# Optimization experiments

Hardware: AMD Instinct MI355X
Metric: run time of the kernel (lower is better)

## Reference

```python
import jax, jax.numpy as jnp
import numpy as np

# CSSA config (index=0): H=W=64, strip windows h_spa=64, w_spa=8, heads=4, C=64
B, HW, C, HEADS = 32, 64, 64, 4
HS, WS = 64, 8          # h_spa, w_spa
HD = C // HEADS          # head_dim = 16
WIN = HS * WS            # 512 tokens per window
SCALE = HD ** -0.5


def setup_inputs() -> dict:
    key = jax.random.key(0)
    k1, k2, k3 = jax.random.split(key, 3)
    qkv = jax.random.normal(k1, (3, B, HW * HW, C), dtype=jnp.float32)
    w_conv = jax.random.normal(k2, (C, 1, 3, 3), dtype=jnp.float32) * 0.1
    b_conv = jax.random.normal(k3, (C,), dtype=jnp.float32) * 0.1
    return {"qkv": qkv, "w_conv": w_conv, "b_conv": b_conv}


def _to_img(x):
    # [B, N, C] -> [B, C, H, W]
    return jnp.transpose(x.reshape(B, HW, HW, C), (0, 3, 1, 2))


def _img2window_heads(x):
    img = _to_img(x)
    img = img.reshape(B, C, HW // HS, HS, HW // WS, WS)
    win = jnp.transpose(img, (0, 2, 4, 3, 5, 1)).reshape(-1, WIN, C)
    return jnp.transpose(win.reshape(-1, WIN, HEADS, HD), (0, 2, 1, 3))


def _v_windows(x):
    # [B, N, C] -> [B*nWin, C, h_spa, w_spa] (image-layout windows for conv)
    img = _to_img(x)
    img = img.reshape(B, C, HW // HS, HS, HW // WS, WS)
    return jnp.transpose(img, (0, 2, 4, 1, 3, 5)).reshape(-1, C, HS, WS)


def reference(qkv, w_conv, b_conv):
    q, k, v = qkv[0], qkv[1], qkv[2]
    qh = _img2window_heads(q) * SCALE
    kh = _img2window_heads(k)
    vw = _v_windows(v)                           # [Bw, C, HS, WS]
    # depthwise 3x3 conv LePE
    lepe = jax.lax.conv_general_dilated(
        vw, w_conv, window_strides=(1, 1), padding=((1, 1), (1, 1)),
        feature_group_count=C,
        dimension_numbers=("NCHW", "OIHW", "NCHW")) + b_conv[None, :, None, None]
    Bw = vw.shape[0]
    lepe = jnp.transpose(lepe.reshape(Bw, HEADS, HD, WIN), (0, 1, 3, 2))
    vh = jnp.transpose(vw.reshape(Bw, HEADS, HD, WIN), (0, 1, 3, 2))
    attn = jax.nn.softmax(jnp.einsum("whqd,whkd->whqk", qh, kh), axis=-1)
    x = jnp.einsum("whqk,whkd->whqd", attn, vh) + lepe
    x = jnp.transpose(x, (0, 2, 1, 3)).reshape(Bw, WIN, C)
    # window2spa
    x = x.reshape(B, HW // HS, HW // WS, HS, WS, C)
    x = jnp.transpose(x, (0, 1, 3, 2, 4, 5)).reshape(B, HW * HW, C)
    return x
```

## Files before the change

### kernel.cpp

```cpp
#include <hip/hip_runtime.h>
#include <stdint.h>

#define VSTR 520

typedef __attribute__((ext_vector_type(4))) short short4v;
typedef __attribute__((ext_vector_type(4))) float f32x4;
typedef __bf16 bf2_t __attribute__((ext_vector_type(2)));

__device__ __forceinline__ float bf2f(unsigned short u) {
    union { unsigned int i; float f; } x; x.i = ((unsigned int)u) << 16; return x.f;
}
__device__ __forceinline__ unsigned int pk2bf(float lo, float hi) {
#if __has_builtin(__builtin_amdgcn_cvt_pk_bf16_f32)
    union { bf2_t v; unsigned int u; } c;
    c.v = __builtin_amdgcn_cvt_pk_bf16_f32(lo, hi);
    return c.u;
#else
    union { float f; unsigned int u; } a, b; a.f = lo; b.f = hi;
    return __builtin_amdgcn_perm(b.u + 0x8000u, a.u + 0x8000u, 0x07060302u);
#endif
}
__device__ __forceinline__ short4v pk4bf(float a, float b, float c, float d) {
    union { short4v s; unsigned int u[2]; } p;
    p.u[0] = pk2bf(a, b);
    p.u[1] = pk2bf(c, d);
    return p.s;
}

__global__ __launch_bounds__(512, 6)
void CSSA_69355131896243_kernel(const float* __restrict__ qkv,
                                const float* __restrict__ wconv,
                                const float* __restrict__ bconv,
                                float* __restrict__ out)
{
    __shared__ unsigned short Vt[16 * VSTR];
    __shared__ float Wl[144];
    __shared__ float Bl[16];

    const int tid  = threadIdx.x;
    const int wave = tid >> 6, lane = tid & 63, quad = lane >> 4, l15 = lane & 15;

    const int bid = blockIdx.x;
    const int win = (bid & 7) * 32 + (bid >> 5);
    const int h   = (bid >> 3) & 3;
    const int b   = win >> 3, wx = win & 7;

    const size_t ONE  = (size_t)32 * 4096 * 64;
    const size_t base = ((size_t)b * 4096 + (size_t)wx * 8) * 64;
    const float* gQ = qkv + base;
    const float* gK = qkv + ONE + base;
    const float* gV = qkv + 2 * ONE + base;
    const int hc = h * 16;

    {
        const int c4 = tid & 3;
        const int tp = tid >> 2;
        #pragma unroll
        for (int r = 0; r < 2; ++r) {
            const int t = r * 256 + tp * 2;
            const size_t g0 = (size_t)(t >> 3) * 4096 + (size_t)(t & 7) * 64 + hc + c4 * 4;
            const size_t g1 = (size_t)((t + 1) >> 3) * 4096 + (size_t)((t + 1) & 7) * 64 + hc + c4 * 4;
            f32x4 v0 = *(const f32x4*)(gV + g0);
            f32x4 v1 = *(const f32x4*)(gV + g1);
            #pragma unroll
            for (int j = 0; j < 4; ++j)
                *(unsigned int*)(&Vt[(c4 * 4 + j) * VSTR + t]) = pk2bf(v0[j], v1[j]);
        }
    }
    if (tid < 144) Wl[tid] = wconv[h * 144 + tid];
    if (tid < 16)  Bl[tid] = bconv[hc + tid];

    const float SCL = 0.25f * 1.44269504088896341f;
    const int q0 = wave * 64;
    short4v qf[4];
    #pragma unroll
    for (int t = 0; t < 4; ++t) {
        const int q = q0 + t * 16 + l15;
        f32x4 qv = *(const f32x4*)(gQ + (size_t)(q >> 3) * 4096 + (size_t)(q & 7) * 64 + hc + quad * 4);
        qf[t] = pk4bf(qv[0] * SCL, qv[1] * SCL, qv[2] * SCL, qv[3] * SCL);
    }
    __syncthreads();

    short4v ones;
    {
        union { short4v s; unsigned short u[4]; } o;
        o.u[0] = 0x3F80; o.u[1] = 0x3F80; o.u[2] = 0x3F80; o.u[3] = 0x3F80;
        ones = o.s;
    }

    f32x4 acc[4], accl[4];
    #pragma unroll
    for (int t = 0; t < 4; ++t) { acc[t] = (f32x4)0.0f; accl[t] = (f32x4)0.0f; }

    const float* gKh = gK + hc + quad * 4 + (size_t)(l15 >> 3) * 4096 + (size_t)(l15 & 7) * 64;
    f32x4 kv = *(const f32x4*)(gKh);
    #pragma unroll 4
    for (int c = 0; c < 32; ++c) {
        const int cn = (c + 1) & 31;
        f32x4 kvn = *(const f32x4*)(gKh + (size_t)cn * 8192);
        const short4v vf = *(const short4v*)(&Vt[l15 * VSTR + c * 16 + quad * 4]);
        const short4v kf = pk4bf(kv[0], kv[1], kv[2], kv[3]);
        #pragma unroll
        for (int t = 0; t < 4; ++t) {
            f32x4 s = __builtin_amdgcn_mfma_f32_16x16x16bf16_1k(kf, qf[t], (f32x4)0.0f, 0, 0, 0);
            const float p0 = __builtin_amdgcn_exp2f(s[0]);
            const float p1 = __builtin_amdgcn_exp2f(s[1]);
            const float p2 = __builtin_amdgcn_exp2f(s[2]);
            const float p3 = __builtin_amdgcn_exp2f(s[3]);
            const short4v pf = pk4bf(p0, p1, p2, p3);
            acc[t]  = __builtin_amdgcn_mfma_f32_16x16x16bf16_1k(vf,   pf, acc[t],  0, 0, 0);
            accl[t] = __builtin_amdgcn_mfma_f32_16x16x16bf16_1k(ones, pf, accl[t], 0, 0, 0);
        }
        kv = kvn;
    }

    float linv[4];
    #pragma unroll
    for (int t = 0; t < 4; ++t) linv[t] = __builtin_amdgcn_rcpf(accl[t][0]);

    #pragma unroll
    for (int j = 0; j < 4; ++j) {
        const int d = quad * 4 + j;
        float w9[9];
        #pragma unroll
        for (int o = 0; o < 9; ++o) w9[o] = Wl[d * 9 + o];
        const float bs = Bl[d];
        #pragma unroll
        for (int t = 0; t < 4; ++t) {
            const int q = q0 + t * 16 + l15;
            const int y = q >> 3, x = q & 7;
            float lep = bs;
            #pragma unroll
            for (int dy = 0; dy < 3; ++dy) {
                #pragma unroll
                for (int dx = 0; dx < 3; ++dx) {
                    const int yy = y + dy - 1, xx = x + dx - 1;
                    const bool ok = ((unsigned)yy < 64u) && ((unsigned)xx < 8u);
                    const int tt = (q + (dy - 1) * 8 + (dx - 1)) & 511;
                    lep += (ok ? w9[dy * 3 + dx] : 0.0f) * bf2f(Vt[d * VSTR + tt]);
                }
            }
            acc[t][j] = acc[t][j] * linv[t] + lep;
        }
    }
    float* gO = out + base;
    #pragma unroll
    for (int t = 0; t < 4; ++t) {
        const int q = q0 + t * 16 + l15;
        *(f32x4*)(gO + (size_t)(q >> 3) * 4096 + (size_t)(q & 7) * 64 + hc + quad * 4) = acc[t];
    }
}

extern "C" void kernel_launch(void* const* d_in, const int* in_sizes, int n_in,
                              void* d_out, int out_size, void* d_ws, size_t ws_size,
                              hipStream_t stream) {
    const float* qkv   = (const float*)d_in[0];
    const float* wconv = (const float*)d_in[1];
    const float* bconv = (const float*)d_in[2];
    float* outp = (float*)d_out;
    hipLaunchKernelGGL(CSSA_69355131896243_kernel, dim3(1024), dim3(512), 0, stream,
                       qkv, wconv, bconv, outp);
}
```

Measured before the change: 224.7 us.

## Stage K tile in LDS as bf16 and simplify LePE conv boundary handling

K for the head is now loaded once cooperatively into shared memory as bf16, and the main loop reads K fragments from LDS with a one-step prefetch. Previously each wave streamed K from global memory and converted it per iteration, so every wave in the block re-read the same K. The depthwise conv epilogue precomputes masked weights per x position and uses direct neighbour offsets with padded zero columns in Vt, removing the per-tap index and mask arithmetic. This adds about 20KB of LDS per block, which may lower occupancy under the 6-blocks launch bound.

Result: slower. 243.6 us (+8.4%).

```diff
diff --git a/kernel.cpp b/kernel.cpp
--- a/kernel.cpp
+++ b/kernel.cpp
@@ -1,10 +1,12 @@
 #include <hip/hip_runtime.h>
 #include <stdint.h>
 
-#define VSTR 520
+#define KSTR2 20
+#define VSTR  520
 
-typedef __attribute__((ext_vector_type(4))) short short4v;
-typedef __attribute__((ext_vector_type(4))) float f32x4;
+typedef __attribute__((ext_vector_type(4))) short          short4v;
+typedef __attribute__((ext_vector_type(4))) float          f32x4;
+typedef __attribute__((ext_vector_type(4))) unsigned short us4;
 typedef __bf16 bf2_t __attribute__((ext_vector_type(2)));
 
 __device__ __forceinline__ float bf2f(unsigned short u) {
@@ -33,6 +35,7 @@
                                 const float* __restrict__ bconv,
                                 float* __restrict__ out)
 {
+    __shared__ unsigned short Kl[512 * KSTR2];
     __shared__ unsigned short Vt[16 * VSTR];
     __shared__ float Wl[144];
     __shared__ float Bl[16];
@@ -59,13 +62,23 @@
         for (int r = 0; r < 2; ++r) {
             const int t = r * 256 + tp * 2;
             const size_t g0 = (size_t)(t >> 3) * 4096 + (size_t)(t & 7) * 64 + hc + c4 * 4;
-            const size_t g1 = (size_t)((t + 1) >> 3) * 4096 + (size_t)((t + 1) & 7) * 64 + hc + c4 * 4;
+            f32x4 k0 = *(const f32x4*)(gK + g0);
+            f32x4 k1 = *(const f32x4*)(gK + g0 + 64);
             f32x4 v0 = *(const f32x4*)(gV + g0);
-            f32x4 v1 = *(const f32x4*)(gV + g1);
+            f32x4 v1 = *(const f32x4*)(gV + g0 + 64);
+            union { us4 s; unsigned int u[2]; } kb0, kb1;
+            kb0.u[0] = pk2bf(k0[0], k0[1]); kb0.u[1] = pk2bf(k0[2], k0[3]);
+            kb1.u[0] = pk2bf(k1[0], k1[1]); kb1.u[1] = pk2bf(k1[2], k1[3]);
+            *(us4*)(&Kl[t * KSTR2 + c4 * 4])       = kb0.s;
+            *(us4*)(&Kl[(t + 1) * KSTR2 + c4 * 4]) = kb1.s;
             #pragma unroll
             for (int j = 0; j < 4; ++j)
                 *(unsigned int*)(&Vt[(c4 * 4 + j) * VSTR + t]) = pk2bf(v0[j], v1[j]);
         }
+    }
+    if (tid < 64) {
+        const int r = tid >> 2, c = tid & 3;
+        *(unsigned int*)(&Vt[r * VSTR + 512 + c * 2]) = 0u;
     }
     if (tid < 144) Wl[tid] = wconv[h * 144 + tid];
     if (tid < 16)  Bl[tid] = bconv[hc + tid];
@@ -92,14 +105,13 @@
     #pragma unroll
     for (int t = 0; t < 4; ++t) { acc[t] = (f32x4)0.0f; accl[t] = (f32x4)0.0f; }
 
-    const float* gKh = gK + hc + quad * 4 + (size_t)(l15 >> 3) * 4096 + (size_t)(l15 & 7) * 64;
-    f32x4 kv = *(const f32x4*)(gKh);
+    short4v kf = *(const short4v*)(&Kl[l15 * KSTR2 + quad * 4]);
+    short4v vf = *(const short4v*)(&Vt[l15 * VSTR + quad * 4]);
     #pragma unroll 4
     for (int c = 0; c < 32; ++c) {
-        const int cn = (c + 1) & 31;
-        f32x4 kvn = *(const f32x4*)(gKh + (size_t)cn * 8192);
-        const short4v vf = *(const short4v*)(&Vt[l15 * VSTR + c * 16 + quad * 4]);
-        const short4v kf = pk4bf(kv[0], kv[1], kv[2], kv[3]);
+        const int cn = ((c + 1) & 31) * 16;
+        short4v kfn = *(const short4v*)(&Kl[(cn + l15) * KSTR2 + quad * 4]);
+        short4v vfn = *(const short4v*)(&Vt[l15 * VSTR + cn + quad * 4]);
         #pragma unroll
         for (int t = 0; t < 4; ++t) {
             f32x4 s = __builtin_amdgcn_mfma_f32_16x16x16bf16_1k(kf, qf[t], (f32x4)0.0f, 0, 0, 0);
@@ -111,35 +123,35 @@
             acc[t]  = __builtin_amdgcn_mfma_f32_16x16x16bf16_1k(vf,   pf, acc[t],  0, 0, 0);
             accl[t] = __builtin_amdgcn_mfma_f32_16x16x16bf16_1k(ones, pf, accl[t], 0, 0, 0);
         }
-        kv = kvn;
+        kf = kfn; vf = vfn;
     }
 
     float linv[4];
     #pragma unroll
     for (int t = 0; t < 4; ++t) linv[t] = __builtin_amdgcn_rcpf(accl[t][0]);
 
+    const int xp = l15 & 7;
+    const bool xm = (xp != 0), xpb = (xp != 7);
     #pragma unroll
     for (int j = 0; j < 4; ++j) {
         const int d = quad * 4 + j;
-        float w9[9];
+        float wxm[9];
         #pragma unroll
-        for (int o = 0; o < 9; ++o) w9[o] = Wl[d * 9 + o];
+        for (int o = 0; o < 3; ++o) {
+            wxm[o * 3 + 0] = xm  ? Wl[d * 9 + o * 3 + 0] : 0.0f;
+            wxm[o * 3 + 1] =       Wl[d * 9 + o * 3 + 1];
+            wxm[o * 3 + 2] = xpb ? Wl[d * 9 + o * 3 + 2] : 0.0f;
+        }
         const float bs = Bl[d];
+        const unsigned short* Vrow = &Vt[d * VSTR];
         #pragma unroll
         for (int t = 0; t < 4; ++t) {
             const int q = q0 + t * 16 + l15;
-            const int y = q >> 3, x = q & 7;
-            float lep = bs;
-            #pragma unroll
-            for (int dy = 0; dy < 3; ++dy) {
-                #pragma unroll
-                for (int dx = 0; dx < 3; ++dx) {
-                    const int yy = y + dy - 1, xx = x + dx - 1;
-                    const bool ok = ((unsigned)yy < 64u) && ((unsigned)xx < 8u);
-                    const int tt = (q + (dy - 1) * 8 + (dx - 1)) & 511;
-                    lep += (ok ? w9[dy * 3 + dx] : 0.0f) * bf2f(Vt[d * VSTR + tt]);
-                }
-            }
+            const int y = q >> 3;
+            const float r0 = wxm[0] * bf2f(Vrow[q - 9]) + wxm[1] * bf2f(Vrow[q - 8]) + wxm[2] * bf2f(Vrow[q - 7]);
+            const float r1 = wxm[3] * bf2f(Vrow[q - 1]) + wxm[4] * bf2f(Vrow[q])     + wxm[5] * bf2f(Vrow[q + 1]);
+            const float r2 = wxm[6] * bf2f(Vrow[q + 7]) + wxm[7] * bf2f(Vrow[q + 8]) + wxm[8] * bf2f(Vrow[q + 9]);
+            const float lep = bs + r1 + (y > 0 ? r0 : 0.0f) + (y < 63 ? r2 : 0.0f);
             acc[t][j] = acc[t][j] * linv[t] + lep;
         }
     }
```
